# Optimization experiments

Measured on AMD Instinct MI355X. Metric: run time of the kernel, lower is better.

The kernel has to match this reference:

```python
import jax, jax.numpy as jnp
import numpy as np

NU = 500000   # num_users
NI = 500000   # num_items
E = 128       # embedding_dim
F = 172       # feature_dim
B = 65536     # number of events in the batch
MSG = 2 * E + F  # GRU input dim = 428


def _gru_cell(x, h, wih, whh, bih, bhh):
    # PyTorch GRUCell: gates ordered (r, z, n)
    gi = x @ wih.T + bih            # [B, 3E]
    gh = h @ whh.T + bhh            # [B, 3E]
    ir, iz, in_ = jnp.split(gi, 3, axis=-1)
    hr, hz, hn = jnp.split(gh, 3, axis=-1)
    r = jax.nn.sigmoid(ir + hr)
    z = jax.nn.sigmoid(iz + hz)
    n = jnp.tanh(in_ + r * hn)
    return (1.0 - z) * n + z * h


def setup_inputs() -> dict:
    key = jax.random.key(0)
    ks = jax.random.split(key, 18)
    s = 0.05  # init scale ~ 1/sqrt(E)
    return {
        "user_ids": jax.random.randint(ks[0], (B,), 0, NU),
        "item_ids": jax.random.randint(ks[1], (B,), 0, NI),
        "timestamps": jax.random.uniform(ks[2], (B,), dtype=jnp.float32) * 1000.0,
        "features": jax.random.normal(ks[3], (B, F), dtype=jnp.float32),
        "query_time": 1200,
        "memory": jax.random.normal(ks[4], (NU + NI, E), dtype=jnp.float32) * 0.1,
        "last_time": jax.random.uniform(ks[5], (NU + NI,), dtype=jnp.float32) * 1000.0,
        "time_w": jax.random.normal(ks[6], (E,), dtype=jnp.float32) * 0.01,  # Linear(1,E,bias=False)
        "u_wih": jax.random.normal(ks[7], (3 * E, MSG), dtype=jnp.float32) * s,
        "u_whh": jax.random.normal(ks[8], (3 * E, E), dtype=jnp.float32) * s,
        "u_bih": jax.random.normal(ks[9], (3 * E,), dtype=jnp.float32) * s,
        "u_bhh": jax.random.normal(ks[10], (3 * E,), dtype=jnp.float32) * s,
        "i_wih": jax.random.normal(ks[11], (3 * E, MSG), dtype=jnp.float32) * s,
        "i_whh": jax.random.normal(ks[12], (3 * E, E), dtype=jnp.float32) * s,
        "i_bih": jax.random.normal(ks[13], (3 * E,), dtype=jnp.float32) * s,
        "i_bhh": jax.random.normal(ks[14], (3 * E,), dtype=jnp.float32) * s,
        "gate_w": jax.random.normal(ks[15], (E, 2 * E), dtype=jnp.float32) * s,
        "gate_b": jnp.zeros((E,), dtype=jnp.float32),
        "pred_w": jax.random.normal(ks[16], (E, E), dtype=jnp.float32) * s,
        "pred_b": jnp.zeros((E,), dtype=jnp.float32),
    }


def reference(user_ids, item_ids, timestamps, features, query_time, memory, last_time,
              time_w, u_wih, u_whh, u_bih, u_bhh, i_wih, i_whh, i_bih, i_bhh,
              gate_w, gate_b, pred_w, pred_b):
    item_nodes = item_ids + NU  # offset items into global node id space
    # per-event gather from node memory
    old_user = memory[user_ids]          # [B, E]
    old_item = memory[item_nodes]        # [B, E]
    last_u = last_time[user_ids]         # [B]
    last_i = last_time[item_nodes]       # [B]

    du = (timestamps - last_u)[:, None]  # [B, 1]
    di = (timestamps - last_i)[:, None]
    # time projection: emb * (1 + Linear(dt))
    proj_user = old_user * (1.0 + du * time_w)
    proj_item = old_item * (1.0 + di * time_w)

    d_query = (jnp.float32(query_time) - last_u)[:, None]
    query_user = old_user * (1.0 + d_query * time_w)

    # peer message mode: user_msg = proj_item, item_msg = proj_user
    user_input = jnp.concatenate([proj_user, proj_item, features], axis=-1)  # [B, MSG]
    item_input = jnp.concatenate([proj_item, proj_user, features], axis=-1)

    new_user = _gru_cell(user_input, old_user, u_wih, u_whh, u_bih, u_bhh)
    new_item = _gru_cell(item_input, old_item, i_wih, i_whh, i_bih, i_bhh)

    # memory gate: g*new + (1-g)*old
    gu = jax.nn.sigmoid(jnp.concatenate([old_user, new_user], axis=-1) @ gate_w.T + gate_b)
    gi = jax.nn.sigmoid(jnp.concatenate([old_item, new_item], axis=-1) @ gate_w.T + gate_b)
    new_user = gu * new_user + (1.0 - gu) * old_user
    new_item = gi * new_item + (1.0 - gi) * old_item

    pred_item_emb = query_user @ pred_w.T + pred_b
    return (pred_item_emb, new_user, new_item)
```

## Files before the change

kernel.cpp:

```cpp
#include <hip/hip_runtime.h>
#include <hip/hip_bf16.h>
#include <cstdint>
#include <cstddef>

#define CNU 500000
#define CB  65536
#define CE  128
#define CF  172
#define EV  64

typedef unsigned short ushort_t;
typedef __attribute__((ext_vector_type(8))) short b8;
typedef __attribute__((ext_vector_type(4))) short b4;
typedef __attribute__((ext_vector_type(4))) float f4;
typedef __attribute__((ext_vector_type(4))) float f32x4;

#define MFMA16(a,b,c) __builtin_amdgcn_mfma_f32_16x16x32_bf16((a),(b),(c),0,0,0)

#define NTL4(p)   __builtin_nontemporal_load((const f32x4*)(p))
#define NTLI(p)   __builtin_nontemporal_load(p)
#define NTS(v, p) __builtin_nontemporal_store((v), (p))

#define FRAG 512
#define U_KT 18
#define U_NT 24
#define U_SZ (U_NT*U_KT*FRAG)
#define PU_OFF 0
#define PI_OFF U_SZ
#define PG_OFF (2*U_SZ)
#define G_SZ (8*8*FRAG)
#define PP_OFF (PG_OFF + G_SZ)
#define P_SZ (8*4*FRAG)

#define SWZ(r, c) ((c) ^ (((r) & 7) << 3))
#define AFRAG(T, r, c) (*(const b8*)&(T)[(r)][SWZ((r), (c))])

__device__ __forceinline__ unsigned pk2bf(float a, float b) {
  __hip_bfloat162 h = __float22bfloat162_rn(make_float2(a, b));
  return *reinterpret_cast<unsigned*>(&h);
}
__device__ __forceinline__ ushort_t f2bf(float f) {
  unsigned u = __float_as_uint(f);
  return (ushort_t)((u + 0x7FFFu + ((u >> 16) & 1u)) >> 16);
}
__device__ __forceinline__ float bf2f(ushort_t h) {
  return __uint_as_float(((unsigned)h) << 16);
}
__device__ __forceinline__ float sigmoid_(float x) { return 1.0f/(1.0f+__expf(-x)); }
__device__ __forceinline__ float tanh_(float x) { float e=__expf(2.0f*x); return 1.0f-2.0f/(e+1.0f); }

struct __align__(16) SLds {
  ushort_t PU[EV][128];
  ushort_t PI[EV][128];
  ushort_t FE[EV][192];
  ushort_t OU[EV][128];
  ushort_t OI[EV][128];
  ushort_t QU[EV][128];
};

extern "C" __global__ void prep_weights(
    const float* __restrict__ u_wih, const float* __restrict__ u_whh,
    const float* __restrict__ i_wih, const float* __restrict__ i_whh,
    const float* __restrict__ gate_w, const float* __restrict__ pred_w,
    ushort_t* __restrict__ ws)
{
  const int stride = gridDim.x * blockDim.x;
  const int tid = blockIdx.x * blockDim.x + threadIdx.x;
  for (int i = tid; i < U_SZ; i += stride) {
    const int nt = i / (U_KT*FRAG);
    const int r1 = i - nt*(U_KT*FRAG);
    const int kt = r1 / FRAG;
    const int e  = r1 - kt*FRAG;
    const int l  = e >> 3, j = e & 7;
    const int n  = nt*16 + (l & 15);
    const int k  = (l >> 4)*8 + j;
    float vu, vi;
    if (kt < 14) {
      const int kk = kt*32 + k;
      vu = (kk < 428) ? u_wih[(size_t)n*428 + kk] : 0.0f;
      vi = (kk < 428) ? i_wih[(size_t)n*428 + kk] : 0.0f;
    } else {
      const int kk = (kt - 14)*32 + k;
      vu = u_whh[(size_t)n*128 + kk];
      vi = i_whh[(size_t)n*128 + kk];
    }
    ws[PU_OFF + i] = f2bf(vu);
    ws[PI_OFF + i] = f2bf(vi);
  }
  for (int i = tid; i < G_SZ; i += stride) {
    const int nt = i / (8*FRAG);
    const int r1 = i - nt*(8*FRAG);
    const int kt = r1 / FRAG;
    const int e  = r1 - kt*FRAG;
    const int l  = e >> 3, j = e & 7;
    const int n  = nt*16 + (l & 15);
    const int kk = kt*32 + (l >> 4)*8 + j;
    ws[PG_OFF + i] = f2bf(gate_w[(size_t)n*256 + kk]);
  }
  for (int i = tid; i < P_SZ; i += stride) {
    const int nt = i / (4*FRAG);
    const int r1 = i - nt*(4*FRAG);
    const int kt = r1 / FRAG;
    const int e  = r1 - kt*FRAG;
    const int l  = e >> 3, j = e & 7;
    const int n  = nt*16 + (l & 15);
    const int kk = kt*32 + (l >> 4)*8 + j;
    ws[PP_OFF + i] = f2bf(pred_w[(size_t)n*128 + kk]);
  }
}

extern "C" __global__ void __launch_bounds__(512, 2)
jodie_main(const int* __restrict__ user_ids, const int* __restrict__ item_ids,
           const float* __restrict__ timestamps, const float* __restrict__ features,
           const int* __restrict__ query_time, const float* __restrict__ memv,
           const float* __restrict__ last_time, const float* __restrict__ time_w,
           const float* __restrict__ u_bih, const float* __restrict__ u_bhh,
           const float* __restrict__ i_bih, const float* __restrict__ i_bhh,
           const float* __restrict__ gate_b, const float* __restrict__ pred_b,
           const ushort_t* __restrict__ ws, float* __restrict__ d_out)
{
  __shared__ SLds s;
  const int t  = threadIdx.x;
  const int e0 = blockIdx.x * EV;

  {
    const int c8 = (t & 15) * 8;
    const float qt = (float)query_time[0];
    const float4 tw0 = *(const float4*)&time_w[c8];
    const float4 tw1 = *(const float4*)&time_w[c8 + 4];
    const float twv[8] = {tw0.x,tw0.y,tw0.z,tw0.w, tw1.x,tw1.y,tw1.z,tw1.w};
#pragma unroll
    for (int ep = 0; ep < 2; ++ep) {
      const int e  = ep*32 + (t >> 4);
      const int ge = e0 + e;
      const int u   = NTLI(&user_ids[ge]);
      const int itn = NTLI(&item_ids[ge]) + CNU;
      const float ts = NTLI(&timestamps[ge]);
      const float lu = NTLI(&last_time[u]);
      const float li = NTLI(&last_time[itn]);
      const float du = ts - lu, di = ts - li, dq = qt - lu;

      const f32x4 ou0 = NTL4(&memv[(size_t)u  *CE + c8]);
      const f32x4 ou1 = NTL4(&memv[(size_t)u  *CE + c8 + 4]);
      const f32x4 oi0 = NTL4(&memv[(size_t)itn*CE + c8]);
      const f32x4 oi1 = NTL4(&memv[(size_t)itn*CE + c8 + 4]);
      const float ouv[8] = {ou0[0],ou0[1],ou0[2],ou0[3], ou1[0],ou1[1],ou1[2],ou1[3]};
      const float oiv[8] = {oi0[0],oi0[1],oi0[2],oi0[3], oi1[0],oi1[1],oi1[2],oi1[3]};

      union U8 { unsigned q[4]; b8 v; };
      U8 xu, xi, hu, hi, qv;
#pragma unroll
      for (int j = 0; j < 8; j += 2) {
        xu.q[j>>1] = pk2bf(ouv[j]*(1.0f + du*twv[j]), ouv[j+1]*(1.0f + du*twv[j+1]));
        xi.q[j>>1] = pk2bf(oiv[j]*(1.0f + di*twv[j]), oiv[j+1]*(1.0f + di*twv[j+1]));
        hu.q[j>>1] = pk2bf(ouv[j], ouv[j+1]);
        hi.q[j>>1] = pk2bf(oiv[j], oiv[j+1]);
        qv.q[j>>1] = pk2bf(ouv[j]*(1.0f + dq*twv[j]), ouv[j+1]*(1.0f + dq*twv[j+1]));
      }
      *(b8*)&s.PU[e][SWZ(e, c8)] = xu.v;
      *(b8*)&s.PI[e][SWZ(e, c8)] = xi.v;
      *(b8*)&s.OU[e][SWZ(e, c8)] = hu.v;
      *(b8*)&s.OI[e][SWZ(e, c8)] = hi.v;
      *(b8*)&s.QU[e][SWZ(e, c8)] = qv.v;
    }
  }
  for (int i = t; i < EV*43; i += 512) {
    const int e = i / 43, q = i - e*43;
    const f32x4 fv = NTL4(&features[(size_t)(e0 + e)*CF + q*4]);
    union { unsigned q2[2]; b4 v; } fb;
    fb.q2[0] = pk2bf(fv[0], fv[1]);
    fb.q2[1] = pk2bf(fv[2], fv[3]);
    *(b4*)&s.FE[e][SWZ(e, q*4)] = fb.v;
  }
  for (int i = t; i < EV*20; i += 512) {
    const int e = i / 20, c = 172 + (i - e*20);
    s.FE[e][SWZ(e, c)] = 0;
  }
  __syncthreads();

  const int wv   = t >> 6, l = t & 63;
  const int lrow = l & 15;
  const int lk   = (l >> 4) * 8;
  const int col  = wv*16 + lrow;

  {
    const float bp = pred_b[col];
    f4 ap[4];
#pragma unroll
    for (int m = 0; m < 4; ++m) ap[m] = (f4){bp,bp,bp,bp};
    const ushort_t* WP = ws + PP_OFF + (size_t)wv*4*FRAG + l*8;
#pragma unroll
    for (int kt = 0; kt < 4; ++kt) {
      b8 fp = *(const b8*)(WP + (size_t)kt*FRAG);
#pragma unroll
      for (int m = 0; m < 4; ++m) {
        b8 a = AFRAG(s.QU, m*16 + lrow, 32*kt + lk);
        ap[m] = MFMA16(a, fp, ap[m]);
      }
    }
#pragma unroll
    for (int m = 0; m < 4; ++m)
#pragma unroll
      for (int r4 = 0; r4 < 4; ++r4) {
        const int row = m*16 + (l >> 4)*4 + r4;
        NTS(ap[m][r4], &d_out[(size_t)(e0 + row)*CE + col]);
      }
  }
  __syncthreads();

  const float bru = u_bih[col]     + u_bhh[col];
  const float bzu = u_bih[col+128] + u_bhh[col+128];
  const float bnu = u_bih[col+256];
  const float bhu = u_bhh[col+256];
  const float bri = i_bih[col]     + i_bhh[col];
  const float bzi = i_bih[col+128] + i_bhh[col+128];
  const float bni = i_bih[col+256];
  const float bhi = i_bhh[col+256];

  f4 aru[4], azu[4], anu[4], ari[4], azi[4], ani[4];
#pragma unroll
  for (int m = 0; m < 4; ++m) {
    aru[m] = (f4){bru,bru,bru,bru};  azu[m] = (f4){bzu,bzu,bzu,bzu};
    anu[m] = (f4){bnu,bnu,bnu,bnu};  ari[m] = (f4){bri,bri,bri,bri};
    azi[m] = (f4){bzi,bzi,bzi,bzi};  ani[m] = (f4){bni,bni,bni,bni};
  }

  const ushort_t* Wru = ws + PU_OFF + (size_t)(wv     )*U_KT*FRAG + l*8;
  const ushort_t* Wzu = ws + PU_OFF + (size_t)(wv +  8)*U_KT*FRAG + l*8;
  const ushort_t* Wnu = ws + PU_OFF + (size_t)(wv + 16)*U_KT*FRAG + l*8;
  const ushort_t* Wri = ws + PI_OFF + (size_t)(wv     )*U_KT*FRAG + l*8;
  const ushort_t* Wzi = ws + PI_OFF + (size_t)(wv +  8)*U_KT*FRAG + l*8;
  const ushort_t* Wni = ws + PI_OFF + (size_t)(wv + 16)*U_KT*FRAG + l*8;

#define GI_STEP(TILE, pf, ktu, kti)                                          \
  {                                                                          \
    b8 a_[4];                                                                \
    _Pragma("unroll")                                                        \
    for (int m = 0; m < 4; ++m) a_[m] = AFRAG(TILE, m*16 + lrow, 32*(pf) + lk); \
    b8 fru = *(const b8*)(Wru + (size_t)(ktu)*FRAG);                         \
    b8 fzu = *(const b8*)(Wzu + (size_t)(ktu)*FRAG);                         \
    b8 fnu = *(const b8*)(Wnu + (size_t)(ktu)*FRAG);                         \
    b8 fri = *(const b8*)(Wri + (size_t)(kti)*FRAG);                         \
    b8 fzi = *(const b8*)(Wzi + (size_t)(kti)*FRAG);                         \
    b8 fni = *(const b8*)(Wni + (size_t)(kti)*FRAG);                         \
    _Pragma("unroll")                                                        \
    for (int m = 0; m < 4; ++m) {                                            \
      aru[m] = MFMA16(a_[m], fru, aru[m]);                                   \
      azu[m] = MFMA16(a_[m], fzu, azu[m]);                                   \
      anu[m] = MFMA16(a_[m], fnu, anu[m]);                                   \
      ari[m] = MFMA16(a_[m], fri, ari[m]);                                   \
      azi[m] = MFMA16(a_[m], fzi, azi[m]);                                   \
      ani[m] = MFMA16(a_[m], fni, ani[m]);                                   \
    }                                                                        \
  }

#pragma unroll
  for (int pf = 0; pf < 4; ++pf) GI_STEP(s.PU, pf, pf, pf + 4)
#pragma unroll
  for (int pf = 0; pf < 4; ++pf) GI_STEP(s.PI, pf, pf + 4, pf)
#pragma unroll
  for (int pf = 0; pf < 6; ++pf) GI_STEP(s.FE, pf, pf + 8, pf + 8)
#undef GI_STEP

  {
    f4 ah[4];
#pragma unroll
    for (int m = 0; m < 4; ++m) ah[m] = (f4){bhu,bhu,bhu,bhu};
#pragma unroll
    for (int kt = 0; kt < 4; ++kt) {
      b8 fr = *(const b8*)(Wru + (size_t)(14+kt)*FRAG);
      b8 fz = *(const b8*)(Wzu + (size_t)(14+kt)*FRAG);
      b8 fn = *(const b8*)(Wnu + (size_t)(14+kt)*FRAG);
#pragma unroll
      for (int m = 0; m < 4; ++m) {
        b8 h = AFRAG(s.OU, m*16 + lrow, 32*kt + lk);
        aru[m] = MFMA16(h, fr, aru[m]);
        azu[m] = MFMA16(h, fz, azu[m]);
        ah[m]  = MFMA16(h, fn, ah[m]);
      }
    }
#pragma unroll
    for (int m = 0; m < 4; ++m)
#pragma unroll
      for (int r4 = 0; r4 < 4; ++r4) {
        const int row = m*16 + (l >> 4)*4 + r4;
        const float rr = sigmoid_(aru[m][r4]);
        const float zz = sigmoid_(azu[m][r4]);
        const float nn = tanh_(anu[m][r4] + rr*ah[m][r4]);
        const float h  = bf2f(s.OU[row][SWZ(row, col)]);
        s.QU[row][SWZ(row, col)] = f2bf((1.0f - zz)*nn + zz*h);
      }
  }
  __syncthreads();

  {
    f4 ah[4];
#pragma unroll
    for (int m = 0; m < 4; ++m) ah[m] = (f4){bhi,bhi,bhi,bhi};
#pragma unroll
    for (int kt = 0; kt < 4; ++kt) {
      b8 fr = *(const b8*)(Wri + (size_t)(14+kt)*FRAG);
      b8 fz = *(const b8*)(Wzi + (size_t)(14+kt)*FRAG);
      b8 fn = *(const b8*)(Wni + (size_t)(14+kt)*FRAG);
#pragma unroll
      for (int m = 0; m < 4; ++m) {
        b8 h = AFRAG(s.OI, m*16 + lrow, 32*kt + lk);
        ari[m] = MFMA16(h, fr, ari[m]);
        azi[m] = MFMA16(h, fz, azi[m]);
        ah[m]  = MFMA16(h, fn, ah[m]);
      }
    }
#pragma unroll
    for (int m = 0; m < 4; ++m)
#pragma unroll
      for (int r4 = 0; r4 < 4; ++r4) {
        const int row = m*16 + (l >> 4)*4 + r4;
        const float rr = sigmoid_(ari[m][r4]);
        const float zz = sigmoid_(azi[m][r4]);
        const float nn = tanh_(ani[m][r4] + rr*ah[m][r4]);
        const float h  = bf2f(s.OI[row][SWZ(row, col)]);
        s.PU[row][SWZ(row, col)] = f2bf((1.0f - zz)*nn + zz*h);
      }
  }
  __syncthreads();

  {
    const float gb = gate_b[col];
    f4 agu[4], agi[4];
#pragma unroll
    for (int m = 0; m < 4; ++m) { agu[m] = (f4){gb,gb,gb,gb}; agi[m] = agu[m]; }
    const ushort_t* WG = ws + PG_OFF + (size_t)wv*8*FRAG + l*8;
#pragma unroll
    for (int kt = 0; kt < 8; ++kt) {
      b8 fg = *(const b8*)(WG + (size_t)kt*FRAG);
#pragma unroll
      for (int m = 0; m < 4; ++m) {
        b8 au = (kt < 4) ? AFRAG(s.OU, m*16 + lrow, 32*kt + lk)
                         : AFRAG(s.QU, m*16 + lrow, 32*(kt-4) + lk);
        b8 ai = (kt < 4) ? AFRAG(s.OI, m*16 + lrow, 32*kt + lk)
                         : AFRAG(s.PU, m*16 + lrow, 32*(kt-4) + lk);
        agu[m] = MFMA16(au, fg, agu[m]);
        agi[m] = MFMA16(ai, fg, agi[m]);
      }
    }
    float* __restrict__ outu = d_out + (size_t)CB*CE;
    float* __restrict__ outi = d_out + (size_t)2*CB*CE;
#pragma unroll
    for (int m = 0; m < 4; ++m)
#pragma unroll
      for (int r4 = 0; r4 < 4; ++r4) {
        const int row = m*16 + (l >> 4)*4 + r4;
        const float gu = sigmoid_(agu[m][r4]);
        const float gi = sigmoid_(agi[m][r4]);
        const float hu  = bf2f(s.OU[row][SWZ(row, col)]);
        const float hpu = bf2f(s.QU[row][SWZ(row, col)]);
        const float hi  = bf2f(s.OI[row][SWZ(row, col)]);
        const float hpi = bf2f(s.PU[row][SWZ(row, col)]);
        NTS(gu*hpu + (1.0f - gu)*hu, &outu[(size_t)(e0 + row)*CE + col]);
        NTS(gi*hpi + (1.0f - gi)*hi, &outi[(size_t)(e0 + row)*CE + col]);
      }
  }
}

extern "C" void kernel_launch(void* const* d_in, const int* in_sizes, int n_in,
                              void* d_out, int out_size, void* d_ws, size_t ws_size,
                              hipStream_t stream) {
  const int*   user_ids   = (const int*)d_in[0];
  const int*   item_ids   = (const int*)d_in[1];
  const float* timestamps = (const float*)d_in[2];
  const float* features   = (const float*)d_in[3];
  const int*   query_time = (const int*)d_in[4];
  const float* memv       = (const float*)d_in[5];
  const float* last_time  = (const float*)d_in[6];
  const float* time_w     = (const float*)d_in[7];
  const float* u_wih = (const float*)d_in[8];
  const float* u_whh = (const float*)d_in[9];
  const float* u_bih = (const float*)d_in[10];
  const float* u_bhh = (const float*)d_in[11];
  const float* i_wih = (const float*)d_in[12];
  const float* i_whh = (const float*)d_in[13];
  const float* i_bih = (const float*)d_in[14];
  const float* i_bhh = (const float*)d_in[15];
  const float* gate_w = (const float*)d_in[16];
  const float* gate_b = (const float*)d_in[17];
  const float* pred_w = (const float*)d_in[18];
  const float* pred_b = (const float*)d_in[19];
  ushort_t* ws = (ushort_t*)d_ws;
  float* out = (float*)d_out;

  prep_weights<<<dim3(256), dim3(256), 0, stream>>>(u_wih, u_whh, i_wih, i_whh,
                                                    gate_w, pred_w, ws);
  jodie_main<<<dim3(CB/EV), dim3(512), 0, stream>>>(user_ids, item_ids, timestamps,
                                                    features, query_time, memv,
                                                    last_time, time_w,
                                                    u_bih, u_bhh, i_bih, i_bhh,
                                                    gate_b, pred_b, ws, out);
}
```

Baseline: 142.9 us.

## Double events per block and apply time projection on the fly from LDS

Raises events per block from 64 to 128 (8 M-tiles per wave), so each weight fragment loaded from global memory feeds twice as many MFMAs. The projected user, item and query embeddings are no longer stored in LDS. They are rebuilt from the old embeddings and per-event time deltas with a bf16 scale just before each MFMA, which frees LDS for the larger tile. The user and item GRUs now run as separate passes with fewer accumulators each, and the new item hidden state reuses the feature buffer. Costs are much higher register pressure (possible spills or lower occupancy), extra ALU for rescaling, one bf16 rounding applied before the scale, and half as many blocks.

```diff
diff --git a/kernel.cpp b/kernel.cpp
--- a/kernel.cpp
+++ b/kernel.cpp
@@ -7,7 +7,8 @@
 #define CB  65536
 #define CE  128
 #define CF  172
-#define EV  64
+#define EV  128
+#define MT  8
 
 typedef unsigned short ushort_t;
 typedef __attribute__((ext_vector_type(8))) short b8;
@@ -49,13 +50,28 @@
 __device__ __forceinline__ float sigmoid_(float x) { return 1.0f/(1.0f+__expf(-x)); }
 __device__ __forceinline__ float tanh_(float x) { float e=__expf(2.0f*x); return 1.0f-2.0f/(e+1.0f); }
 
+__device__ __forceinline__ b8 scale8(b8 x, float d, f32x4 t0, f32x4 t1) {
+  union { ushort_t u[8]; unsigned q[4]; b8 v; } in, out;
+  in.v = x;
+  const float tt[8] = {t0[0],t0[1],t0[2],t0[3], t1[0],t1[1],t1[2],t1[3]};
+#pragma unroll
+  for (int j = 0; j < 4; ++j) {
+    float a = bf2f(in.u[2*j]);
+    float b = bf2f(in.u[2*j+1]);
+    a = fmaf(a, d*tt[2*j],   a);
+    b = fmaf(b, d*tt[2*j+1], b);
+    out.q[j] = pk2bf(a, b);
+  }
+  return out.v;
+}
+
 struct __align__(16) SLds {
-  ushort_t PU[EV][128];
-  ushort_t PI[EV][128];
-  ushort_t FE[EV][192];
   ushort_t OU[EV][128];
   ushort_t OI[EV][128];
-  ushort_t QU[EV][128];
+  ushort_t FE[EV][192];
+  ushort_t HU[EV][128];
+  float TW[128];
+  float DU[EV], DI[EV], DQ[EV];
 };
 
 extern "C" __global__ void prep_weights(
@@ -120,17 +136,16 @@
            const ushort_t* __restrict__ ws, float* __restrict__ d_out)
 {
   __shared__ SLds s;
+  ushort_t (*HI)[128] = (ushort_t (*)[128])(&s.FE[0][0]);
   const int t  = threadIdx.x;
   const int e0 = blockIdx.x * EV;
 
+  if (t < 32) *(float4*)&s.TW[t*4] = *(const float4*)&time_w[t*4];
   {
     const int c8 = (t & 15) * 8;
     const float qt = (float)query_time[0];
-    const float4 tw0 = *(const float4*)&time_w[c8];
-    const float4 tw1 = *(const float4*)&time_w[c8 + 4];
-    const float twv[8] = {tw0.x,tw0.y,tw0.z,tw0.w, tw1.x,tw1.y,tw1.z,tw1.w};
-#pragma unroll
-    for (int ep = 0; ep < 2; ++ep) {
+#pragma unroll
+    for (int ep = 0; ep < 4; ++ep) {
       const int e  = ep*32 + (t >> 4);
       const int ge = e0 + e;
       const int u   = NTLI(&user_ids[ge]);
@@ -138,30 +153,22 @@
       const float ts = NTLI(&timestamps[ge]);
       const float lu = NTLI(&last_time[u]);
       const float li = NTLI(&last_time[itn]);
-      const float du = ts - lu, di = ts - li, dq = qt - lu;
-
+      if ((t & 15) == 0) {
+        s.DU[e] = ts - lu;
+        s.DI[e] = ts - li;
+        s.DQ[e] = qt - lu;
+      }
       const f32x4 ou0 = NTL4(&memv[(size_t)u  *CE + c8]);
       const f32x4 ou1 = NTL4(&memv[(size_t)u  *CE + c8 + 4]);
       const f32x4 oi0 = NTL4(&memv[(size_t)itn*CE + c8]);
       const f32x4 oi1 = NTL4(&memv[(size_t)itn*CE + c8 + 4]);
-      const float ouv[8] = {ou0[0],ou0[1],ou0[2],ou0[3], ou1[0],ou1[1],ou1[2],ou1[3]};
-      const float oiv[8] = {oi0[0],oi0[1],oi0[2],oi0[3], oi1[0],oi1[1],oi1[2],oi1[3]};
-
-      union U8 { unsigned q[4]; b8 v; };
-      U8 xu, xi, hu, hi, qv;
-#pragma unroll
-      for (int j = 0; j < 8; j += 2) {
-        xu.q[j>>1] = pk2bf(ouv[j]*(1.0f + du*twv[j]), ouv[j+1]*(1.0f + du*twv[j+1]));
-        xi.q[j>>1] = pk2bf(oiv[j]*(1.0f + di*twv[j]), oiv[j+1]*(1.0f + di*twv[j+1]));
-        hu.q[j>>1] = pk2bf(ouv[j], ouv[j+1]);
-        hi.q[j>>1] = pk2bf(oiv[j], oiv[j+1]);
-        qv.q[j>>1] = pk2bf(ouv[j]*(1.0f + dq*twv[j]), ouv[j+1]*(1.0f + dq*twv[j+1]));
-      }
-      *(b8*)&s.PU[e][SWZ(e, c8)] = xu.v;
-      *(b8*)&s.PI[e][SWZ(e, c8)] = xi.v;
+      union { unsigned q[4]; b8 v; } hu, hi;
+      hu.q[0] = pk2bf(ou0[0], ou0[1]);  hu.q[1] = pk2bf(ou0[2], ou0[3]);
+      hu.q[2] = pk2bf(ou1[0], ou1[1]);  hu.q[3] = pk2bf(ou1[2], ou1[3]);
+      hi.q[0] = pk2bf(oi0[0], oi0[1]);  hi.q[1] = pk2bf(oi0[2], oi0[3]);
+      hi.q[2] = pk2bf(oi1[0], oi1[1]);  hi.q[3] = pk2bf(oi1[2], oi1[3]);
       *(b8*)&s.OU[e][SWZ(e, c8)] = hu.v;
       *(b8*)&s.OI[e][SWZ(e, c8)] = hi.v;
-      *(b8*)&s.QU[e][SWZ(e, c8)] = qv.v;
     }
   }
   for (int i = t; i < EV*43; i += 512) {
@@ -183,179 +190,242 @@
   const int lk   = (l >> 4) * 8;
   const int col  = wv*16 + lrow;
 
-  {
-    const float bp = pred_b[col];
-    f4 ap[4];
-#pragma unroll
-    for (int m = 0; m < 4; ++m) ap[m] = (f4){bp,bp,bp,bp};
-    const ushort_t* WP = ws + PP_OFF + (size_t)wv*4*FRAG + l*8;
-#pragma unroll
-    for (int kt = 0; kt < 4; ++kt) {
-      b8 fp = *(const b8*)(WP + (size_t)kt*FRAG);
-#pragma unroll
-      for (int m = 0; m < 4; ++m) {
-        b8 a = AFRAG(s.QU, m*16 + lrow, 32*kt + lk);
-        ap[m] = MFMA16(a, fp, ap[m]);
-      }
-    }
-#pragma unroll
-    for (int m = 0; m < 4; ++m)
-#pragma unroll
-      for (int r4 = 0; r4 < 4; ++r4) {
-        const int row = m*16 + (l >> 4)*4 + r4;
-        NTS(ap[m][r4], &d_out[(size_t)(e0 + row)*CE + col]);
-      }
-  }
-  __syncthreads();
-
-  const float bru = u_bih[col]     + u_bhh[col];
-  const float bzu = u_bih[col+128] + u_bhh[col+128];
-  const float bnu = u_bih[col+256];
-  const float bhu = u_bhh[col+256];
-  const float bri = i_bih[col]     + i_bhh[col];
-  const float bzi = i_bih[col+128] + i_bhh[col+128];
-  const float bni = i_bih[col+256];
-  const float bhi = i_bhh[col+256];
-
-  f4 aru[4], azu[4], anu[4], ari[4], azi[4], ani[4];
-#pragma unroll
-  for (int m = 0; m < 4; ++m) {
-    aru[m] = (f4){bru,bru,bru,bru};  azu[m] = (f4){bzu,bzu,bzu,bzu};
-    anu[m] = (f4){bnu,bnu,bnu,bnu};  ari[m] = (f4){bri,bri,bri,bri};
-    azi[m] = (f4){bzi,bzi,bzi,bzi};  ani[m] = (f4){bni,bni,bni,bni};
-  }
-
   const ushort_t* Wru = ws + PU_OFF + (size_t)(wv     )*U_KT*FRAG + l*8;
   const ushort_t* Wzu = ws + PU_OFF + (size_t)(wv +  8)*U_KT*FRAG + l*8;
   const ushort_t* Wnu = ws + PU_OFF + (size_t)(wv + 16)*U_KT*FRAG + l*8;
   const ushort_t* Wri = ws + PI_OFF + (size_t)(wv     )*U_KT*FRAG + l*8;
   const ushort_t* Wzi = ws + PI_OFF + (size_t)(wv +  8)*U_KT*FRAG + l*8;
   const ushort_t* Wni = ws + PI_OFF + (size_t)(wv + 16)*U_KT*FRAG + l*8;
-
-#define GI_STEP(TILE, pf, ktu, kti)                                          \
-  {                                                                          \
-    b8 a_[4];                                                                \
-    _Pragma("unroll")                                                        \
-    for (int m = 0; m < 4; ++m) a_[m] = AFRAG(TILE, m*16 + lrow, 32*(pf) + lk); \
-    b8 fru = *(const b8*)(Wru + (size_t)(ktu)*FRAG);                         \
-    b8 fzu = *(const b8*)(Wzu + (size_t)(ktu)*FRAG);                         \
-    b8 fnu = *(const b8*)(Wnu + (size_t)(ktu)*FRAG);                         \
-    b8 fri = *(const b8*)(Wri + (size_t)(kti)*FRAG);                         \
-    b8 fzi = *(const b8*)(Wzi + (size_t)(kti)*FRAG);                         \
-    b8 fni = *(const b8*)(Wni + (size_t)(kti)*FRAG);                         \
-    _Pragma("unroll")                                                        \
-    for (int m = 0; m < 4; ++m) {                                            \
-      aru[m] = MFMA16(a_[m], fru, aru[m]);                                   \
-      azu[m] = MFMA16(a_[m], fzu, azu[m]);                                   \
-      anu[m] = MFMA16(a_[m], fnu, anu[m]);                                   \
-      ari[m] = MFMA16(a_[m], fri, ari[m]);                                   \
-      azi[m] = MFMA16(a_[m], fzi, azi[m]);                                   \
-      ani[m] = MFMA16(a_[m], fni, ani[m]);                                   \
-    }                                                                        \
-  }
-
-#pragma unroll
-  for (int pf = 0; pf < 4; ++pf) GI_STEP(s.PU, pf, pf, pf + 4)
-#pragma unroll
-  for (int pf = 0; pf < 4; ++pf) GI_STEP(s.PI, pf, pf + 4, pf)
-#pragma unroll
-  for (int pf = 0; pf < 6; ++pf) GI_STEP(s.FE, pf, pf + 8, pf + 8)
-#undef GI_STEP
+  const ushort_t* WP  = ws + PP_OFF + (size_t)wv*4*FRAG + l*8;
+  const ushort_t* WG  = ws + PG_OFF + (size_t)wv*8*FRAG + l*8;
 
   {
-    f4 ah[4];
-#pragma unroll
-    for (int m = 0; m < 4; ++m) ah[m] = (f4){bhu,bhu,bhu,bhu};
-#pragma unroll
-    for (int kt = 0; kt < 4; ++kt) {
-      b8 fr = *(const b8*)(Wru + (size_t)(14+kt)*FRAG);
-      b8 fz = *(const b8*)(Wzu + (size_t)(14+kt)*FRAG);
-      b8 fn = *(const b8*)(Wnu + (size_t)(14+kt)*FRAG);
-#pragma unroll
-      for (int m = 0; m < 4; ++m) {
-        b8 h = AFRAG(s.OU, m*16 + lrow, 32*kt + lk);
-        aru[m] = MFMA16(h, fr, aru[m]);
-        azu[m] = MFMA16(h, fz, azu[m]);
-        ah[m]  = MFMA16(h, fn, ah[m]);
-      }
-    }
-#pragma unroll
-    for (int m = 0; m < 4; ++m)
+    const float bp = pred_b[col];
+    f4 ap[MT];
+#pragma unroll
+    for (int m = 0; m < MT; ++m) ap[m] = (f4){bp,bp,bp,bp};
+#pragma unroll
+    for (int kt = 0; kt < 4; ++kt) {
+      b8 fp = *(const b8*)(WP + (size_t)kt*FRAG);
+      const f32x4 t0 = *(const f32x4*)&s.TW[32*kt + lk];
+      const f32x4 t1 = *(const f32x4*)&s.TW[32*kt + lk + 4];
+#pragma unroll
+      for (int m = 0; m < MT; ++m) {
+        b8 a = scale8(AFRAG(s.OU, m*16 + lrow, 32*kt + lk), s.DQ[m*16 + lrow], t0, t1);
+        ap[m] = MFMA16(a, fp, ap[m]);
+      }
+    }
+#pragma unroll
+    for (int m = 0; m < MT; ++m)
 #pragma unroll
       for (int r4 = 0; r4 < 4; ++r4) {
         const int row = m*16 + (l >> 4)*4 + r4;
-        const float rr = sigmoid_(aru[m][r4]);
-        const float zz = sigmoid_(azu[m][r4]);
-        const float nn = tanh_(anu[m][r4] + rr*ah[m][r4]);
-        const float h  = bf2f(s.OU[row][SWZ(row, col)]);
-        s.QU[row][SWZ(row, col)] = f2bf((1.0f - zz)*nn + zz*h);
-      }
-  }
-  __syncthreads();
+        NTS(ap[m][r4], &d_out[(size_t)(e0 + row)*CE + col]);
+      }
+  }
 
   {
-    f4 ah[4];
-#pragma unroll
-    for (int m = 0; m < 4; ++m) ah[m] = (f4){bhi,bhi,bhi,bhi};
-#pragma unroll
-    for (int kt = 0; kt < 4; ++kt) {
-      b8 fr = *(const b8*)(Wri + (size_t)(14+kt)*FRAG);
-      b8 fz = *(const b8*)(Wzi + (size_t)(14+kt)*FRAG);
-      b8 fn = *(const b8*)(Wni + (size_t)(14+kt)*FRAG);
-#pragma unroll
-      for (int m = 0; m < 4; ++m) {
-        b8 h = AFRAG(s.OI, m*16 + lrow, 32*kt + lk);
-        ari[m] = MFMA16(h, fr, ari[m]);
-        azi[m] = MFMA16(h, fz, azi[m]);
-        ah[m]  = MFMA16(h, fn, ah[m]);
-      }
-    }
-#pragma unroll
-    for (int m = 0; m < 4; ++m)
+    const float br = u_bih[col]     + u_bhh[col];
+    const float bz = u_bih[col+128] + u_bhh[col+128];
+    const float bn = u_bih[col+256];
+    const float bh = u_bhh[col+256];
+    f4 ar[MT], az[MT], an8[MT], ah[MT];
+#pragma unroll
+    for (int m = 0; m < MT; ++m) {
+      ar[m] = (f4){br,br,br,br};  az[m] = (f4){bz,bz,bz,bz};
+      an8[m] = (f4){bn,bn,bn,bn}; ah[m] = (f4){bh,bh,bh,bh};
+    }
+#pragma unroll
+    for (int kt = 0; kt < 4; ++kt) {
+      b8 fr = *(const b8*)(Wru + (size_t)kt*FRAG);
+      b8 fz = *(const b8*)(Wzu + (size_t)kt*FRAG);
+      b8 fn = *(const b8*)(Wnu + (size_t)kt*FRAG);
+      const f32x4 t0 = *(const f32x4*)&s.TW[32*kt + lk];
+      const f32x4 t1 = *(const f32x4*)&s.TW[32*kt + lk + 4];
+#pragma unroll
+      for (int m = 0; m < MT; ++m) {
+        b8 a = scale8(AFRAG(s.OU, m*16 + lrow, 32*kt + lk), s.DU[m*16 + lrow], t0, t1);
+        ar[m] = MFMA16(a, fr, ar[m]);
+        az[m] = MFMA16(a, fz, az[m]);
+        an8[m] = MFMA16(a, fn, an8[m]);
+      }
+    }
+#pragma unroll
+    for (int kt = 0; kt < 4; ++kt) {
+      b8 fr = *(const b8*)(Wru + (size_t)(kt+4)*FRAG);
+      b8 fz = *(const b8*)(Wzu + (size_t)(kt+4)*FRAG);
+      b8 fn = *(const b8*)(Wnu + (size_t)(kt+4)*FRAG);
+      const f32x4 t0 = *(const f32x4*)&s.TW[32*kt + lk];
+      const f32x4 t1 = *(const f32x4*)&s.TW[32*kt + lk + 4];
+#pragma unroll
+      for (int m = 0; m < MT; ++m) {
+        b8 a = scale8(AFRAG(s.OI, m*16 + lrow, 32*kt + lk), s.DI[m*16 + lrow], t0, t1);
+        ar[m] = MFMA16(a, fr, ar[m]);
+        az[m] = MFMA16(a, fz, az[m]);
+        an8[m] = MFMA16(a, fn, an8[m]);
+      }
+    }
+#pragma unroll
+    for (int kt = 0; kt < 6; ++kt) {
+      b8 fr = *(const b8*)(Wru + (size_t)(kt+8)*FRAG);
+      b8 fz = *(const b8*)(Wzu + (size_t)(kt+8)*FRAG);
+      b8 fn = *(const b8*)(Wnu + (size_t)(kt+8)*FRAG);
+#pragma unroll
+      for (int m = 0; m < MT; ++m) {
+        b8 a = AFRAG(s.FE, m*16 + lrow, 32*kt + lk);
+        ar[m] = MFMA16(a, fr, ar[m]);
+        az[m] = MFMA16(a, fz, az[m]);
+        an8[m] = MFMA16(a, fn, an8[m]);
+      }
+    }
+#pragma unroll
+    for (int kt = 0; kt < 4; ++kt) {
+      b8 fr = *(const b8*)(Wru + (size_t)(kt+14)*FRAG);
+      b8 fz = *(const b8*)(Wzu + (size_t)(kt+14)*FRAG);
+      b8 fn = *(const b8*)(Wnu + (size_t)(kt+14)*FRAG);
+#pragma unroll
+      for (int m = 0; m < MT; ++m) {
+        b8 h = AFRAG(s.OU, m*16 + lrow, 32*kt + lk);
+        ar[m] = MFMA16(h, fr, ar[m]);
+        az[m] = MFMA16(h, fz, az[m]);
+        ah[m] = MFMA16(h, fn, ah[m]);
+      }
+    }
+#pragma unroll
+    for (int m = 0; m < MT; ++m)
 #pragma unroll
       for (int r4 = 0; r4 < 4; ++r4) {
         const int row = m*16 + (l >> 4)*4 + r4;
-        const float rr = sigmoid_(ari[m][r4]);
-        const float zz = sigmoid_(azi[m][r4]);
-        const float nn = tanh_(ani[m][r4] + rr*ah[m][r4]);
+        const float rr = sigmoid_(ar[m][r4]);
+        const float zz = sigmoid_(az[m][r4]);
+        const float nn = tanh_(an8[m][r4] + rr*ah[m][r4]);
+        const float h  = bf2f(s.OU[row][SWZ(row, col)]);
+        s.HU[row][SWZ(row, col)] = f2bf((1.0f - zz)*nn + zz*h);
+      }
+  }
+
+  {
+    const float br = i_bih[col]     + i_bhh[col];
+    const float bz = i_bih[col+128] + i_bhh[col+128];
+    const float bn = i_bih[col+256];
+    const float bh = i_bhh[col+256];
+    f4 ar[MT], az[MT], an8[MT], ah[MT];
+#pragma unroll
+    for (int m = 0; m < MT; ++m) {
+      ar[m] = (f4){br,br,br,br};  az[m] = (f4){bz,bz,bz,bz};
+      an8[m] = (f4){bn,bn,bn,bn}; ah[m] = (f4){bh,bh,bh,bh};
+    }
+#pragma unroll
+    for (int kt = 0; kt < 4; ++kt) {
+      b8 fr = *(const b8*)(Wri + (size_t)kt*FRAG);
+      b8 fz = *(const b8*)(Wzi + (size_t)kt*FRAG);
+      b8 fn = *(const b8*)(Wni + (size_t)kt*FRAG);
+      const f32x4 t0 = *(const f32x4*)&s.TW[32*kt + lk];
+      const f32x4 t1 = *(const f32x4*)&s.TW[32*kt + lk + 4];
+#pragma unroll
+      for (int m = 0; m < MT; ++m) {
+        b8 a = scale8(AFRAG(s.OI, m*16 + lrow, 32*kt + lk), s.DI[m*16 + lrow], t0, t1);
+        ar[m] = MFMA16(a, fr, ar[m]);
+        az[m] = MFMA16(a, fz, az[m]);
+        an8[m] = MFMA16(a, fn, an8[m]);
+      }
+    }
+#pragma unroll
+    for (int kt = 0; kt < 4; ++kt) {
+      b8 fr = *(const b8*)(Wri + (size_t)(kt+4)*FRAG);
+      b8 fz = *(const b8*)(Wzi + (size_t)(kt+4)*FRAG);
+      b8 fn = *(const b8*)(Wni + (size_t)(kt+4)*FRAG);
+      const f32x4 t0 = *(const f32x4*)&s.TW[32*kt + lk];
+      const f32x4 t1 = *(const f32x4*)&s.TW[32*kt + lk + 4];
+#pragma unroll
+      for (int m = 0; m < MT; ++m) {
+        b8 a = scale8(AFRAG(s.OU, m*16 + lrow, 32*kt + lk), s.DU[m*16 + lrow], t0, t1);
+        ar[m] = MFMA16(a, fr, ar[m]);
+        az[m] = MFMA16(a, fz, az[m]);
+        an8[m] = MFMA16(a, fn, an8[m]);
+      }
+    }
+#pragma unroll
+    for (int kt = 0; kt < 6; ++kt) {
+      b8 fr = *(const b8*)(Wri + (size_t)(kt+8)*FRAG);
+      b8 fz = *(const b8*)(Wzi + (size_t)(kt+8)*FRAG);
+      b8 fn = *(const b8*)(Wni + (size_t)(kt+8)*FRAG);
+#pragma unroll
+      for (int m = 0; m < MT; ++m) {
+        b8 a = AFRAG(s.FE, m*16 + lrow, 32*kt + lk);
+        ar[m] = MFMA16(a, fr, ar[m]);
+        az[m] = MFMA16(a, fz, az[m]);
+        an8[m] = MFMA16(a, fn, an8[m]);
+      }
+    }
+#pragma unroll
+    for (int kt = 0; kt < 4; ++kt) {
+      b8 fr = *(const b8*)(Wri + (size_t)(kt+14)*FRAG);
+      b8 fz = *(const b8*)(Wzi + (size_t)(kt+14)*FRAG);
+      b8 fn = *(const b8*)(Wni + (size_t)(kt+14)*FRAG);
+#pragma unroll
+      for (int m = 0; m < MT; ++m) {
+        b8 h = AFRAG(s.OI, m*16 + lrow, 32*kt + lk);
+        ar[m] = MFMA16(h, fr, ar[m]);
+        az[m] = MFMA16(h, fz, az[m]);
+        ah[m] = MFMA16(h, fn, ah[m]);
+      }
+    }
+    __syncthreads();
+#pragma unroll
+    for (int m = 0; m < MT; ++m)
+#pragma unroll
+      for (int r4 = 0; r4 < 4; ++r4) {
+        const int row = m*16 + (l >> 4)*4 + r4;
+        const float rr = sigmoid_(ar[m][r4]);
+        const float zz = sigmoid_(az[m][r4]);
+        const float nn = tanh_(an8[m][r4] + rr*ah[m][r4]);
         const float h  = bf2f(s.OI[row][SWZ(row, col)]);
-        s.PU[row][SWZ(row, col)] = f2bf((1.0f - zz)*nn + zz*h);
+        HI[row][SWZ(row, col)] = f2bf((1.0f - zz)*nn + zz*h);
       }
   }
   __syncthreads();
 
   {
     const float gb = gate_b[col];
-    f4 agu[4], agi[4];
-#pragma unroll
-    for (int m = 0; m < 4; ++m) { agu[m] = (f4){gb,gb,gb,gb}; agi[m] = agu[m]; }
-    const ushort_t* WG = ws + PG_OFF + (size_t)wv*8*FRAG + l*8;
-#pragma unroll
-    for (int kt = 0; kt < 8; ++kt) {
+    f4 agu[MT], agi[MT];
+#pragma unroll
+    for (int m = 0; m < MT; ++m) { agu[m] = (f4){gb,gb,gb,gb}; agi[m] = agu[m]; }
+#pragma unroll
+    for (int kt = 0; kt < 4; ++kt) {
       b8 fg = *(const b8*)(WG + (size_t)kt*FRAG);
 #pragma unroll
-      for (int m = 0; m < 4; ++m) {
-        b8 au = (kt < 4) ? AFRAG(s.OU, m*16 + lrow, 32*kt + lk)
-                         : AFRAG(s.QU, m*16 + lrow, 32*(kt-4) + lk);
-        b8 ai = (kt < 4) ? AFRAG(s.OI, m*16 + lrow, 32*kt + lk)
-                         : AFRAG(s.PU, m*16 + lrow, 32*(kt-4) + lk);
+      for (int m = 0; m < MT; ++m) {
+        b8 au = AFRAG(s.OU, m*16 + lrow, 32*kt + lk);
+        b8 ai = AFRAG(s.OI, m*16 + lrow, 32*kt + lk);
         agu[m] = MFMA16(au, fg, agu[m]);
         agi[m] = MFMA16(ai, fg, agi[m]);
       }
     }
+#pragma unroll
+    for (int kt = 0; kt < 4; ++kt) {
+      b8 fg = *(const b8*)(WG + (size_t)(kt+4)*FRAG);
+#pragma unroll
+      for (int m = 0; m < MT; ++m) {
+        b8 au = AFRAG(s.HU, m*16 + lrow, 32*kt + lk);
+        b8 ai = AFRAG(HI,   m*16 + lrow, 32*kt + lk);
+        agu[m] = MFMA16(au, fg, agu[m]);
+        agi[m] = MFMA16(ai, fg, agi[m]);
+      }
+    }
     float* __restrict__ outu = d_out + (size_t)CB*CE;
     float* __restrict__ outi = d_out + (size_t)2*CB*CE;
 #pragma unroll
-    for (int m = 0; m < 4; ++m)
+    for (int m = 0; m < MT; ++m)
 #pragma unroll
       for (int r4 = 0; r4 < 4; ++r4) {
         const int row = m*16 + (l >> 4)*4 + r4;
         const float gu = sigmoid_(agu[m][r4]);
         const float gi = sigmoid_(agi[m][r4]);
         const float hu  = bf2f(s.OU[row][SWZ(row, col)]);
-        const float hpu = bf2f(s.QU[row][SWZ(row, col)]);
+        const float hpu = bf2f(s.HU[row][SWZ(row, col)]);
         const float hi  = bf2f(s.OI[row][SWZ(row, col)]);
-        const float hpi = bf2f(s.PU[row][SWZ(row, col)]);
+        const float hpi = bf2f(HI[row][SWZ(row, col)]);
         NTS(gu*hpu + (1.0f - gu)*hu, &outu[(size_t)(e0 + row)*CE + col]);
         NTS(gi*hpi + (1.0f - gi)*hi, &outi[(size_t)(e0 + row)*CE + col]);
       }
```

Measured after the change: 255.2 us. 78.6% more time.
